# Optimization experiments

Measured on AMD Instinct MI355X. Metric: run time of the kernel, lower is better.

Reference implementation:

```python
import jax, jax.numpy as jnp
from jax import lax
import numpy as np

D_IN, D_H, M_BANK = 1024, 512, 100


def setup_inputs() -> dict:
    key = jax.random.key(0)
    ks = jax.random.split(key, 12)
    B, T = 128, 256
    s = 0.01
    return {
        "hidden_frames": jax.random.normal(ks[0], (B, T, D_IN), jnp.float32),
        # hidden_to_content: Linear(hidden+input -> hidden)
        "W_c": jax.random.normal(ks[1], (D_H + D_IN, D_H), jnp.float32) * s,
        "b_c": jnp.zeros((D_H,), jnp.float32),
        # read_prob: Linear(hidden+input -> memory_bank_size)
        "W_rp": jax.random.normal(ks[2], (D_H + D_IN, M_BANK), jnp.float32) * s,
        "b_rp": jnp.zeros((M_BANK,), jnp.float32),
        # write_prob: Linear(hidden+input -> memory_bank_size)
        "W_wp": jax.random.normal(ks[3], (D_H + D_IN, M_BANK), jnp.float32) * s,
        "b_wp": jnp.zeros((M_BANK,), jnp.float32),
        # RNN cell params (init: normal(0, 0.01), bias zero)
        "Wxh": jax.random.normal(ks[4], (D_IN, D_H), jnp.float32) * s,
        "Wrh": jax.random.normal(ks[5], (D_H, D_H), jnp.float32) * s,
        "Whh": jax.random.normal(ks[6], (D_H, D_H), jnp.float32) * s,
        "bh": jnp.zeros((D_H,), jnp.float32),
        "nImg": 256,
    }


def reference(hidden_frames, W_c, b_c, W_rp, b_rp, W_wp, b_wp, Wxh, Wrh, Whh, bh, nImg):
    B = hidden_frames.shape[0]
    H = Wxh.shape[1]
    M = W_rp.shape[1]

    def step(carry, x_t):
        # x_t: (B, D_in); h: (B, H); mem: (B, M, H)
        h, mem = carry
        xh = jnp.concatenate([x_t, h], axis=-1)            # (B, D_in+H)
        ar = jax.nn.softmax(xh @ W_rp + b_rp, axis=-1)     # (B, M) read weights
        r = jnp.einsum('bm,bmh->bh', ar, mem)              # (B, H) read vector
        h_new = jax.nn.relu(x_t @ Wxh + r @ Wrh + h @ Whh + bh)
        c = jax.nn.relu(xh @ W_c + b_c)                    # (B, H) write content
        aw = jax.nn.softmax(xh @ W_wp + b_wp, axis=-1)[:, :, None]  # (B, M, 1)
        mem = aw * c[:, None, :] + (1.0 - aw) * mem        # gated blend overwrite
        return (h_new, mem), h_new

    xs = jnp.swapaxes(hidden_frames[:, :nImg, :], 0, 1)    # (T, B, D_in)
    h0 = jnp.zeros((B, H), hidden_frames.dtype)
    mem0 = jnp.zeros((B, M, H), hidden_frames.dtype)
    _, hs = lax.scan(step, (h0, mem0), xs)                 # hs: (T, B, H)
    return jnp.swapaxes(hs, 0, 1)                          # (B, T, H)
```

## Files before the change

kernel.cpp:

```cpp
#include <hip/hip_runtime.h>

#define D_IN   1024
#define D_H    512
#define M_BANK 100
#define BATCH  128
#define NCOL   1224
#define NPAD   1280
#define KTOT   1536
#define KSH    4

typedef unsigned short u16;
typedef __attribute__((ext_vector_type(8))) short s16x8;
typedef __attribute__((ext_vector_type(4))) float f32x4;

__device__ __forceinline__ u16 f2bf(float f) {
  union { float f; unsigned int u; } v;
  v.f = f;
  unsigned int r = (v.u + 0x7FFFu + ((v.u >> 16) & 1u)) >> 16;
  return (u16)r;
}
__device__ __forceinline__ float bf2f(u16 b) {
  union { unsigned int u; float f; } v;
  v.u = ((unsigned int)b) << 16;
  return v.f;
}

__global__ void k_prep_w(const float* __restrict__ W_c,
                         const float* __restrict__ W_rp,
                         const float* __restrict__ W_wp,
                         const float* __restrict__ Wxh,
                         const float* __restrict__ Whh,
                         u16* __restrict__ W_bt) {
  const int j = blockIdx.x;
  const int k = blockIdx.y * 256 + threadIdx.x;
  float v = 0.f;
  if (j < 100)       v = W_rp[(size_t)k * M_BANK + j];
  else if (j < 200)  v = W_wp[(size_t)k * M_BANK + (j - 100)];
  else if (j < 712)  v = W_c[(size_t)k * D_H + (j - 200)];
  else if (j < NCOL) v = (k < D_IN) ? Wxh[(size_t)k * D_H + (j - 712)]
                                    : Whh[(size_t)(k - D_IN) * D_H + (j - 712)];
  W_bt[(size_t)j * KTOT + k] = f2bf(v);
}

__global__ void k_prep_wrh(const float* __restrict__ Wrh,
                           u16* __restrict__ Wrh_bf) {
  const int i = blockIdx.x * 256 + threadIdx.x;
  Wrh_bf[i] = f2bf(Wrh[i]);
}

__global__ void k_zx_mfma(const float* __restrict__ frames,
                          const u16* __restrict__ W_bt,
                          float* __restrict__ zx,
                          int t0, int CH, int lgCH, int TF) {
  __shared__ u16 Asb[64][40];
  __shared__ u16 Bsb[64][40];
  const int tid  = threadIdx.x;
  const int lane = tid & 63;
  const int wid  = tid >> 6;
  const int wm   = wid >> 1, wn = wid & 1;
  const int j0 = blockIdx.x * 64;
  const int r0 = blockIdx.y * 64;
  const int srow = tid >> 2;
  const int skk  = (tid & 3) * 8;
  const int gr = r0 + srow;
  const int b  = gr >> lgCH;
  const int tc = gr & (CH - 1);
  const float* arow = &frames[((size_t)b * TF + t0 + tc) * D_IN];
  const u16*   brow = &W_bt[(size_t)(j0 + srow) * KTOT];

  f32x4 a00 = {0.f, 0.f, 0.f, 0.f}, a01 = {0.f, 0.f, 0.f, 0.f};
  f32x4 a10 = {0.f, 0.f, 0.f, 0.f}, a11 = {0.f, 0.f, 0.f, 0.f};

  for (int k0 = 0; k0 < D_IN; k0 += 32) {
    const float4 v0 = *reinterpret_cast<const float4*>(&arow[k0 + skk]);
    const float4 v1 = *reinterpret_cast<const float4*>(&arow[k0 + skk + 4]);
    s16x8 a8;
    a8[0] = (short)f2bf(v0.x); a8[1] = (short)f2bf(v0.y);
    a8[2] = (short)f2bf(v0.z); a8[3] = (short)f2bf(v0.w);
    a8[4] = (short)f2bf(v1.x); a8[5] = (short)f2bf(v1.y);
    a8[6] = (short)f2bf(v1.z); a8[7] = (short)f2bf(v1.w);
    *reinterpret_cast<s16x8*>(&Asb[srow][skk]) = a8;
    *reinterpret_cast<s16x8*>(&Bsb[srow][skk]) =
        *reinterpret_cast<const s16x8*>(&brow[k0 + skk]);
    __syncthreads();
    const int ka = (lane >> 4) * 8;
    const s16x8 af0 = *reinterpret_cast<s16x8*>(&Asb[wm * 32 + (lane & 15)][ka]);
    const s16x8 af1 = *reinterpret_cast<s16x8*>(&Asb[wm * 32 + 16 + (lane & 15)][ka]);
    const s16x8 bf0 = *reinterpret_cast<s16x8*>(&Bsb[wn * 32 + (lane & 15)][ka]);
    const s16x8 bf1 = *reinterpret_cast<s16x8*>(&Bsb[wn * 32 + 16 + (lane & 15)][ka]);
    a00 = __builtin_amdgcn_mfma_f32_16x16x32_bf16(af0, bf0, a00, 0, 0, 0);
    a01 = __builtin_amdgcn_mfma_f32_16x16x32_bf16(af0, bf1, a01, 0, 0, 0);
    a10 = __builtin_amdgcn_mfma_f32_16x16x32_bf16(af1, bf0, a10, 0, 0, 0);
    a11 = __builtin_amdgcn_mfma_f32_16x16x32_bf16(af1, bf1, a11, 0, 0, 0);
    __syncthreads();
  }
  const int rb = r0 + wm * 32 + (lane >> 4) * 4;
  const int cb = j0 + wn * 32 + (lane & 15);
#define STORE_ACC(A, MF, NF)                                             \
  {                                                                      \
    _Pragma("unroll")                                                    \
    for (int reg = 0; reg < 4; ++reg)                                    \
      zx[(size_t)(rb + MF * 16 + reg) * NPAD + cb + NF * 16] = A[reg];   \
  }
  STORE_ACC(a00, 0, 0) STORE_ACC(a01, 0, 1) STORE_ACC(a10, 1, 0) STORE_ACC(a11, 1, 1)
#undef STORE_ACC
}

__global__ void __launch_bounds__(256)
k_zh_mfma(const u16* __restrict__ h_bf,
          const u16* __restrict__ W_bt,
          float* __restrict__ zhp) {
  __shared__ u16 Asb[64][136];
  __shared__ u16 Bsb[64][136];
  const int tid  = threadIdx.x;
  const int lane = tid & 63;
  const int wid  = tid >> 6;
  const int wm   = wid >> 1, wn = wid & 1;
  const int j0 = blockIdx.x * 64;
  const int r0 = blockIdx.y * 64;
  const int kp = blockIdx.z;
  const int srow = tid >> 2;
  const int sseg = (tid & 3) * 32;
  const u16* arow = &h_bf[(size_t)(r0 + srow) * D_H + kp * 128 + sseg];
  const u16* brow = &W_bt[(size_t)(j0 + srow) * KTOT + D_IN + kp * 128 + sseg];

  #pragma unroll
  for (int i = 0; i < 4; ++i) {
    *reinterpret_cast<s16x8*>(&Asb[srow][sseg + i * 8]) =
        *reinterpret_cast<const s16x8*>(&arow[i * 8]);
    *reinterpret_cast<s16x8*>(&Bsb[srow][sseg + i * 8]) =
        *reinterpret_cast<const s16x8*>(&brow[i * 8]);
  }
  __syncthreads();

  f32x4 a00 = {0.f, 0.f, 0.f, 0.f}, a01 = {0.f, 0.f, 0.f, 0.f};
  f32x4 a10 = {0.f, 0.f, 0.f, 0.f}, a11 = {0.f, 0.f, 0.f, 0.f};
  const int la = lane & 15;
  #pragma unroll
  for (int kk = 0; kk < 4; ++kk) {
    const int ka = kk * 32 + (lane >> 4) * 8;
    const s16x8 af0 = *reinterpret_cast<s16x8*>(&Asb[wm * 32 + la][ka]);
    const s16x8 af1 = *reinterpret_cast<s16x8*>(&Asb[wm * 32 + 16 + la][ka]);
    const s16x8 bf0 = *reinterpret_cast<s16x8*>(&Bsb[wn * 32 + la][ka]);
    const s16x8 bf1 = *reinterpret_cast<s16x8*>(&Bsb[wn * 32 + 16 + la][ka]);
    a00 = __builtin_amdgcn_mfma_f32_16x16x32_bf16(af0, bf0, a00, 0, 0, 0);
    a01 = __builtin_amdgcn_mfma_f32_16x16x32_bf16(af0, bf1, a01, 0, 0, 0);
    a10 = __builtin_amdgcn_mfma_f32_16x16x32_bf16(af1, bf0, a10, 0, 0, 0);
    a11 = __builtin_amdgcn_mfma_f32_16x16x32_bf16(af1, bf1, a11, 0, 0, 0);
  }
  const int rb = r0 + wm * 32 + (lane >> 4) * 4;
  const int cb = j0 + wn * 32 + (lane & 15);
  float* zp = &zhp[(size_t)kp * BATCH * NPAD];
#define STORE_ACC(A, MF, NF)                                             \
  {                                                                      \
    _Pragma("unroll")                                                    \
    for (int reg = 0; reg < 4; ++reg)                                    \
      zp[(size_t)(rb + MF * 16 + reg) * NPAD + cb + NF * 16] = A[reg];   \
  }
  STORE_ACC(a00, 0, 0) STORE_ACC(a01, 0, 1) STORE_ACC(a10, 1, 0) STORE_ACC(a11, 1, 1)
#undef STORE_ACC
}

__global__ void __launch_bounds__(512)
k_phase2(const float* __restrict__ zx,
         const float* __restrict__ zhp,
         const u16* __restrict__ Wrh_bf,
         const float* __restrict__ b_rp,
         const float* __restrict__ b_wp,
         const float* __restrict__ b_c,
         const float* __restrict__ bh,
         u16* __restrict__ M2b,
         float* __restrict__ out,
         u16* __restrict__ h_bf,
         int t, int tc, int CH, int T) {
  __shared__ float ar_s[2][M_BANK];
  __shared__ float aw_s[2][M_BANK];
  __shared__ float c_s[2][D_H];
  __shared__ float red[2][16][32][4];
  __shared__ float smx[2][2][2];
  __shared__ float ssm[2][2][2];
  const int tid  = threadIdx.x;
  const int ba   = tid >> 8;
  const int lane = tid & 31;
  const int p    = blockIdx.x;
  const int b0   = blockIdx.y * 2;
  const int b_g  = b0 + ba;
  const int s0   = p * 128 + lane * 4;
  const bool hz  = (t > 0);
  const size_t zxrow = (size_t)(b_g * CH + tc) * NPAD;

  {
    const int u     = tid & 255;
    const int which = u >> 7;
    const int m     = u & 127;
    const int wv    = (u >> 6) & 1;
    float l = -1e30f;
    if (m < M_BANK) {
      const int col = which * 100 + m;
      l = (which ? b_wp[m] : b_rp[m]) + zx[zxrow + col];
      if (hz) {
        #pragma unroll
        for (int q = 0; q < KSH; ++q)
          l += zhp[(size_t)(q * BATCH + b_g) * NPAD + col];
      }
    }
    float mx = l;
    #pragma unroll
    for (int o = 32; o; o >>= 1) mx = fmaxf(mx, __shfl_xor(mx, o, 64));
    if ((tid & 63) == 0) smx[ba][which][wv] = mx;
    __syncthreads();
    mx = fmaxf(smx[ba][which][0], smx[ba][which][1]);
    const float e = (m < M_BANK) ? __expf(l - mx) : 0.f;
    float s = e;
    #pragma unroll
    for (int o = 32; o; o >>= 1) s += __shfl_xor(s, o, 64);
    if ((tid & 63) == 0) ssm[ba][which][wv] = s;
    __syncthreads();
    s = ssm[ba][which][0] + ssm[ba][which][1];
    if (m < M_BANK) {
      const float a = e / s;
      if (which) aw_s[ba][m] = a;
      else       ar_s[ba][m] = a;
    }
  }
  for (int idx = tid; idx < 2 * D_H; idx += 512) {
    const int bb  = idx >> 9;
    const int k   = idx & 511;
    const int bg2 = b0 + bb;
    float v = b_c[k] + zx[(size_t)(bg2 * CH + tc) * NPAD + 200 + k];
    if (hz) {
      #pragma unroll
      for (int q = 0; q < KSH; ++q)
        v += zhp[(size_t)(q * BATCH + bg2) * NPAD + 200 + k];
    }
    c_s[bb][k] = fmaxf(v, 0.f);
  }
  __syncthreads();

  const int mg    = (tid >> 5) & 7;
  const int mcnt  = (mg < 4) ? 13 : 12;
  const int mbase = (mg < 4) ? mg * 13 : 52 + (mg - 4) * 12;
  u16* mp = &M2b[((size_t)b_g * M_BANK + mbase) * D_H + s0];
  ushort4 m2v[13];
  #pragma unroll
  for (int mm = 0; mm < 13; ++mm)
    if (mm < mcnt)
      m2v[mm] = *reinterpret_cast<const ushort4*>(mp + (size_t)mm * D_H);

  {
    const int g = tid >> 5;
    float cwa[4] = {};
    float cwb[4] = {};
    const int kbase = g * 32;
    #pragma unroll 8
    for (int kk = 0; kk < 32; ++kk) {
      const int k = kbase + kk;
      const ushort4 w4 = *reinterpret_cast<const ushort4*>(&Wrh_bf[(size_t)k * D_H + s0]);
      const float w0 = bf2f(w4.x), w1 = bf2f(w4.y), w2 = bf2f(w4.z), w3 = bf2f(w4.w);
      const float ca = c_s[0][k];
      const float cb = c_s[1][k];
      cwa[0] += ca * w0; cwa[1] += ca * w1; cwa[2] += ca * w2; cwa[3] += ca * w3;
      cwb[0] += cb * w0; cwb[1] += cb * w1; cwb[2] += cb * w2; cwb[3] += cb * w3;
    }
    #pragma unroll
    for (int j = 0; j < 4; ++j) {
      red[0][g][lane][j] = cwa[j];
      red[1][g][lane][j] = cwb[j];
    }
  }
  __syncthreads();
  float cw[4] = {};
  #pragma unroll
  for (int gg = 0; gg < 16; ++gg)
    #pragma unroll
    for (int j = 0; j < 4; ++j) cw[j] += red[ba][gg][lane][j];
  __syncthreads();

  float racc[4] = {};
  #pragma unroll
  for (int mm = 0; mm < 13; ++mm) {
    if (mm < mcnt) {
      const int m = mbase + mm;
      const ushort4 v4 = m2v[mm];
      const float v0 = bf2f(v4.x), v1 = bf2f(v4.y), v2 = bf2f(v4.z), v3 = bf2f(v4.w);
      const float a = ar_s[ba][m];
      const float w = aw_s[ba][m];
      racc[0] += a * v0; racc[1] += a * v1; racc[2] += a * v2; racc[3] += a * v3;
      ushort4 nv;
      nv.x = f2bf(w * cw[0] + (1.f - w) * v0);
      nv.y = f2bf(w * cw[1] + (1.f - w) * v1);
      nv.z = f2bf(w * cw[2] + (1.f - w) * v2);
      nv.w = f2bf(w * cw[3] + (1.f - w) * v3);
      *reinterpret_cast<ushort4*>(mp + (size_t)mm * D_H) = nv;
    }
  }
  #pragma unroll
  for (int j = 0; j < 4; ++j) red[ba][mg][lane][j] = racc[j];
  __syncthreads();

  if ((tid & 255) < 32) {
    float ph[4];
    const float4 vb = *reinterpret_cast<const float4*>(&bh[s0]);
    const float4 px = *reinterpret_cast<const float4*>(&zx[zxrow + 712 + s0]);
    ph[0] = vb.x + px.x; ph[1] = vb.y + px.y;
    ph[2] = vb.z + px.z; ph[3] = vb.w + px.w;
    #pragma unroll
    for (int gg = 0; gg < 8; ++gg)
      #pragma unroll
      for (int j = 0; j < 4; ++j) ph[j] += red[ba][gg][lane][j];
    if (hz) {
      #pragma unroll
      for (int q = 0; q < KSH; ++q) {
        const float4 pz = *reinterpret_cast<const float4*>(
            &zhp[(size_t)(q * BATCH + b_g) * NPAD + 712 + s0]);
        ph[0] += pz.x; ph[1] += pz.y; ph[2] += pz.z; ph[3] += pz.w;
      }
    }
    float4 h;
    h.x = fmaxf(ph[0], 0.f); h.y = fmaxf(ph[1], 0.f);
    h.z = fmaxf(ph[2], 0.f); h.w = fmaxf(ph[3], 0.f);
    *reinterpret_cast<float4*>(&out[((size_t)b_g * T + t) * D_H + s0]) = h;
    ushort4 hb;
    hb.x = f2bf(h.x); hb.y = f2bf(h.y); hb.z = f2bf(h.z); hb.w = f2bf(h.w);
    *reinterpret_cast<ushort4*>(&h_bf[(size_t)b_g * D_H + s0]) = hb;
  }
}

extern "C" void kernel_launch(void* const* d_in, const int* in_sizes, int n_in,
                              void* d_out, int out_size, void* d_ws, size_t ws_size,
                              hipStream_t stream) {
  const float* frames = (const float*)d_in[0];
  const float* W_c    = (const float*)d_in[1];
  const float* b_c    = (const float*)d_in[2];
  const float* W_rp   = (const float*)d_in[3];
  const float* b_rp   = (const float*)d_in[4];
  const float* W_wp   = (const float*)d_in[5];
  const float* b_wp   = (const float*)d_in[6];
  const float* Wxh    = (const float*)d_in[7];
  const float* Wrh    = (const float*)d_in[8];
  const float* Whh    = (const float*)d_in[9];
  const float* bh     = (const float*)d_in[10];
  float* out = (float*)d_out;

  const int TF = in_sizes[0] / (BATCH * D_IN);
  const int T  = out_size / (BATCH * D_H);

  const size_t M2B_FL   = (size_t)BATCH * M_BANK * D_H / 2;
  const size_t ZHP_FL   = (size_t)KSH * BATCH * NPAD;
  const size_t WBT_FL   = (size_t)NPAD * KTOT / 2;
  const size_t WRH_FL   = (size_t)D_H * D_H / 2;
  const size_t HBF_FL   = (size_t)BATCH * D_H / 2;

  u16*   M2b = (u16*)d_ws;
  float* zhp = (float*)d_ws + M2B_FL;
  float* zx  = zhp + ZHP_FL;

  int CH = 64, lgCH = 6;
  while (CH > 1 &&
         ((M2B_FL + ZHP_FL + WBT_FL + WRH_FL + HBF_FL +
           (size_t)BATCH * CH * NPAD) * sizeof(float) > ws_size ||
          (T % CH) != 0)) {
    CH >>= 1; --lgCH;
  }

  u16* W_bt   = (u16*)(zx + (size_t)BATCH * CH * NPAD);
  u16* Wrh_bf = W_bt + (size_t)NPAD * KTOT;
  u16* h_bf   = Wrh_bf + (size_t)D_H * D_H;

  hipMemsetAsync(M2b, 0, M2B_FL * sizeof(float), stream);
  k_prep_w<<<dim3(NPAD, KTOT / 256), 256, 0, stream>>>(W_c, W_rp, W_wp, Wxh, Whh, W_bt);
  k_prep_wrh<<<dim3(D_H * D_H / 256), 256, 0, stream>>>(Wrh, Wrh_bf);

  for (int t0 = 0; t0 < T; t0 += CH) {
    k_zx_mfma<<<dim3(NPAD / 64, BATCH * CH / 64), 256, 0, stream>>>(
        frames, W_bt, zx, t0, CH, lgCH, TF);
    for (int t = t0; t < t0 + CH; ++t) {
      if (t > 0)
        k_zh_mfma<<<dim3(NPAD / 64, BATCH / 64, KSH), 256, 0, stream>>>(h_bf, W_bt, zhp);
      k_phase2<<<dim3(D_H / 128, BATCH / 2), 512, 0, stream>>>(
          zx, zhp, Wrh_bf, b_rp, b_wp, b_c, bh, M2b, out, h_bf, t, t - t0, CH, T);
    }
  }
}
```

Before: 4.242 ms.

## Halve zh split-K partials and overlap softmax with content computation

The recurrent zh GEMM now uses two K-splits of 256 instead of four of 128. This doubles the per-block shared-memory tiles and MFMA loop, and halves both the partial buffers and the per-step reduction reads in the step kernel. In the step kernel, the first 256 threads compute both batch rows' softmaxes while the other 256 compute the write content, which removes the duplicated softmax work per half-block. The trade-off is fewer zh blocks, so less parallelism, and larger LDS use per block.

```diff
diff --git a/kernel.cpp b/kernel.cpp
--- a/kernel.cpp
+++ b/kernel.cpp
@@ -7,7 +7,7 @@
 #define NCOL   1224
 #define NPAD   1280
 #define KTOT   1536
-#define KSH    4
+#define KSH    2
 
 typedef unsigned short u16;
 typedef __attribute__((ext_vector_type(8))) short s16x8;
@@ -110,8 +110,8 @@
 k_zh_mfma(const u16* __restrict__ h_bf,
           const u16* __restrict__ W_bt,
           float* __restrict__ zhp) {
-  __shared__ u16 Asb[64][136];
-  __shared__ u16 Bsb[64][136];
+  __shared__ u16 Asb[64][264];
+  __shared__ u16 Bsb[64][264];
   const int tid  = threadIdx.x;
   const int lane = tid & 63;
   const int wid  = tid >> 6;
@@ -120,12 +120,12 @@
   const int r0 = blockIdx.y * 64;
   const int kp = blockIdx.z;
   const int srow = tid >> 2;
-  const int sseg = (tid & 3) * 32;
-  const u16* arow = &h_bf[(size_t)(r0 + srow) * D_H + kp * 128 + sseg];
-  const u16* brow = &W_bt[(size_t)(j0 + srow) * KTOT + D_IN + kp * 128 + sseg];
-
-  #pragma unroll
-  for (int i = 0; i < 4; ++i) {
+  const int sseg = (tid & 3) * 64;
+  const u16* arow = &h_bf[(size_t)(r0 + srow) * D_H + kp * 256 + sseg];
+  const u16* brow = &W_bt[(size_t)(j0 + srow) * KTOT + D_IN + kp * 256 + sseg];
+
+  #pragma unroll
+  for (int i = 0; i < 8; ++i) {
     *reinterpret_cast<s16x8*>(&Asb[srow][sseg + i * 8]) =
         *reinterpret_cast<const s16x8*>(&arow[i * 8]);
     *reinterpret_cast<s16x8*>(&Bsb[srow][sseg + i * 8]) =
@@ -137,7 +137,7 @@
   f32x4 a10 = {0.f, 0.f, 0.f, 0.f}, a11 = {0.f, 0.f, 0.f, 0.f};
   const int la = lane & 15;
   #pragma unroll
-  for (int kk = 0; kk < 4; ++kk) {
+  for (int kk = 0; kk < 8; ++kk) {
     const int ka = kk * 32 + (lane >> 4) * 8;
     const s16x8 af0 = *reinterpret_cast<s16x8*>(&Asb[wm * 32 + la][ka]);
     const s16x8 af1 = *reinterpret_cast<s16x8*>(&Asb[wm * 32 + 16 + la][ka]);
@@ -189,51 +189,81 @@
   const bool hz  = (t > 0);
   const size_t zxrow = (size_t)(b_g * CH + tc) * NPAD;
 
-  {
-    const int u     = tid & 255;
-    const int which = u >> 7;
-    const int m     = u & 127;
-    const int wv    = (u >> 6) & 1;
-    float l = -1e30f;
-    if (m < M_BANK) {
-      const int col = which * 100 + m;
-      l = (which ? b_wp[m] : b_rp[m]) + zx[zxrow + col];
+  const int sm_which = tid >> 7;
+  const int sm_m     = tid & 127;
+  const int sm_wv    = (tid >> 6) & 1;
+  float lv0 = -1e30f, lv1 = -1e30f;
+  if (tid < 256) {
+    if (sm_m < M_BANK) {
+      const int col = sm_which * 100 + sm_m;
+      const float bias = sm_which ? b_wp[sm_m] : b_rp[sm_m];
+      lv0 = bias + zx[(size_t)((b0 + 0) * CH + tc) * NPAD + col];
+      lv1 = bias + zx[(size_t)((b0 + 1) * CH + tc) * NPAD + col];
+      if (hz) {
+        #pragma unroll
+        for (int q = 0; q < KSH; ++q) {
+          lv0 += zhp[(size_t)(q * BATCH + b0 + 0) * NPAD + col];
+          lv1 += zhp[(size_t)(q * BATCH + b0 + 1) * NPAD + col];
+        }
+      }
+    }
+    float mx0 = lv0, mx1 = lv1;
+    #pragma unroll
+    for (int o = 32; o; o >>= 1) {
+      mx0 = fmaxf(mx0, __shfl_xor(mx0, o, 64));
+      mx1 = fmaxf(mx1, __shfl_xor(mx1, o, 64));
+    }
+    if ((tid & 63) == 0) {
+      smx[0][sm_which][sm_wv] = mx0;
+      smx[1][sm_which][sm_wv] = mx1;
+    }
+  } else {
+    for (int idx = tid - 256; idx < 2 * D_H; idx += 256) {
+      const int bb  = idx >> 9;
+      const int k   = idx & 511;
+      const int bg2 = b0 + bb;
+      float v = b_c[k] + zx[(size_t)(bg2 * CH + tc) * NPAD + 200 + k];
       if (hz) {
         #pragma unroll
         for (int q = 0; q < KSH; ++q)
-          l += zhp[(size_t)(q * BATCH + b_g) * NPAD + col];
+          v += zhp[(size_t)(q * BATCH + bg2) * NPAD + 200 + k];
       }
-    }
-    float mx = l;
+      c_s[bb][k] = fmaxf(v, 0.f);
+    }
+  }
+  __syncthreads();
+
+  float e0 = 0.f, e1 = 0.f;
+  if (tid < 256) {
+    const float mx0 = fmaxf(smx[0][sm_which][0], smx[0][sm_which][1]);
+    const float mx1 = fmaxf(smx[1][sm_which][0], smx[1][sm_which][1]);
+    if (sm_m < M_BANK) {
+      e0 = __expf(lv0 - mx0);
+      e1 = __expf(lv1 - mx1);
+    }
+    float s0 = e0, s1 = e1;
     #pragma unroll
-    for (int o = 32; o; o >>= 1) mx = fmaxf(mx, __shfl_xor(mx, o, 64));
-    if ((tid & 63) == 0) smx[ba][which][wv] = mx;
-    __syncthreads();
-    mx = fmaxf(smx[ba][which][0], smx[ba][which][1]);
-    const float e = (m < M_BANK) ? __expf(l - mx) : 0.f;
-    float s = e;
-    #pragma unroll
-    for (int o = 32; o; o >>= 1) s += __shfl_xor(s, o, 64);
-    if ((tid & 63) == 0) ssm[ba][which][wv] = s;
-    __syncthreads();
-    s = ssm[ba][which][0] + ssm[ba][which][1];
-    if (m < M_BANK) {
-      const float a = e / s;
-      if (which) aw_s[ba][m] = a;
-      else       ar_s[ba][m] = a;
-    }
-  }
-  for (int idx = tid; idx < 2 * D_H; idx += 512) {
-    const int bb  = idx >> 9;
-    const int k   = idx & 511;
-    const int bg2 = b0 + bb;
-    float v = b_c[k] + zx[(size_t)(bg2 * CH + tc) * NPAD + 200 + k];
-    if (hz) {
-      #pragma unroll
-      for (int q = 0; q < KSH; ++q)
-        v += zhp[(size_t)(q * BATCH + bg2) * NPAD + 200 + k];
-    }
-    c_s[bb][k] = fmaxf(v, 0.f);
+    for (int o = 32; o; o >>= 1) {
+      s0 += __shfl_xor(s0, o, 64);
+      s1 += __shfl_xor(s1, o, 64);
+    }
+    if ((tid & 63) == 0) {
+      ssm[0][sm_which][sm_wv] = s0;
+      ssm[1][sm_which][sm_wv] = s1;
+    }
+  }
+  __syncthreads();
+
+  if (tid < 256 && sm_m < M_BANK) {
+    const float s0 = ssm[0][sm_which][0] + ssm[0][sm_which][1];
+    const float s1 = ssm[1][sm_which][0] + ssm[1][sm_which][1];
+    if (sm_which) {
+      aw_s[0][sm_m] = e0 / s0;
+      aw_s[1][sm_m] = e1 / s1;
+    } else {
+      ar_s[0][sm_m] = e0 / s0;
+      ar_s[1][sm_m] = e1 / s1;
+    }
   }
   __syncthreads();
 
```

Measured after the change: 4.557 ms. +7.4%, slower.
